# Optimization experiments

Measured on AMD Instinct MI355X. Metric: run time of the kernel, lower is better.

The kernel has to match this reference:

```python
import jax, jax.numpy as jnp
import numpy as np

B = 16384           # number of visits (segments)
EMB = 128           # embedding dim (hardcoded in module)
HID = 64            # hidden layer size
DIAG_LEN, PROC_LEN, MED_LEN = 2000, 1500, 153


def setup_inputs() -> dict:
    key = jax.random.key(0)
    ks = jax.random.split(key, 12)
    diag_codes = jax.random.randint(ks[0], (262144,), 0, DIAG_LEN)
    diag_seg = jnp.sort(jax.random.randint(ks[1], (262144,), 0, B))
    proc_codes = jax.random.randint(ks[2], (131072,), 0, PROC_LEN)
    proc_seg = jnp.sort(jax.random.randint(ks[3], (131072,), 0, B))
    med_codes = jax.random.randint(ks[4], (196608,), 0, MED_LEN)
    med_seg = jnp.sort(jax.random.randint(ks[5], (196608,), 0, B))
    diag_table = jax.random.normal(ks[6], (DIAG_LEN, EMB), dtype=jnp.float32)
    proc_table = jax.random.normal(ks[7], (PROC_LEN, EMB), dtype=jnp.float32)
    med_table = jax.random.normal(ks[8], (MED_LEN, EMB), dtype=jnp.float32)
    W1 = jax.random.normal(ks[9], (3 * EMB, HID), dtype=jnp.float32) * 0.05
    b1 = jnp.zeros((HID,), dtype=jnp.float32)
    W2 = jax.random.normal(ks[10], (HID, MED_LEN), dtype=jnp.float32) * 0.1
    b2 = jnp.zeros((MED_LEN,), dtype=jnp.float32)
    return {
        "diag_codes": diag_codes, "diag_seg": diag_seg,
        "proc_codes": proc_codes, "proc_seg": proc_seg,
        "med_codes": med_codes, "med_seg": med_seg,
        "diag_table": diag_table, "proc_table": proc_table, "med_table": med_table,
        "W1": W1, "b1": b1, "W2": W2, "b2": b2,
    }


def _embed_sum(table, codes, seg):
    # gather [N, EMB] then segment-sum to [B, EMB] (== per-visit sum of embeddings)
    return jax.ops.segment_sum(table[codes], seg, num_segments=B)


def reference(diag_codes, diag_seg, proc_codes, proc_seg, med_codes, med_seg,
              diag_table, proc_table, med_table, W1, b1, W2, b2):
    e_diag = _embed_sum(diag_table, diag_codes, diag_seg)   # [B, 128]
    e_proc = _embed_sum(proc_table, proc_codes, proc_seg)   # [B, 128]
    e_med = _embed_sum(med_table, med_codes, med_seg)       # [B, 128]
    x = jnp.concatenate([e_diag, e_proc, e_med], axis=1)    # [B, 384]
    h = jax.nn.relu(x @ W1 + b1)                            # [B, 64]
    return jax.nn.sigmoid(h @ W2 + b2)                      # [B, med_len]
```

## Files before the change

kernel.cpp:

```cpp
#include <hip/hip_runtime.h>
#include <hip/hip_bf16.h>

#define NVIS 16384
#define EMB 128
#define HID 64
#define MED 153
#define K1 384
#define VPB 16
#define NTHR 512
#define NBLK (NVIS / VPB)
#define CAPD 640
#define CAPP 384
#define CAPM 512
#define CAPT (CAPD + CAPP + CAPM)

#define W1F_OFF 0u
#define W2F_OFF 49152u
#define DIAG_OFF 69632u
#define PROC_OFF 581632u
#define MED_OFF  965632u
#define WS_NEED  1004800u

#define TQ_D 32000
#define TQ_P 24000
#define TQ_M 2448
#define TQ_ALL (TQ_D + TQ_P + TQ_M)
#define NW1F 3072
#define NW2F 1280
#define PREP_THREADS (TQ_ALL + NW1F + NW2F)
#define PREP_BLOCKS ((PREP_THREADS + 255) / 256)

typedef float f32x4 __attribute__((ext_vector_type(4)));
typedef short s16x8 __attribute__((ext_vector_type(8)));
typedef unsigned int u32;
typedef unsigned int u32x4 __attribute__((ext_vector_type(4)));

__device__ __forceinline__ unsigned short f2bf(float f) {
  union { float f; unsigned u; } v; v.f = f;
  unsigned r = v.u + 0x7FFFu + ((v.u >> 16) & 1u);
  return (unsigned short)(r >> 16);
}

__device__ __forceinline__ void acc8(u32x4 t, float& a0, float& a1, float& a2, float& a3,
                                               float& a4, float& a5, float& a6, float& a7) {
  union { unsigned u; float f; } c;
  c.u = t[0] << 16;          a0 += c.f;
  c.u = t[0] & 0xFFFF0000u;  a1 += c.f;
  c.u = t[1] << 16;          a2 += c.f;
  c.u = t[1] & 0xFFFF0000u;  a3 += c.f;
  c.u = t[2] << 16;          a4 += c.f;
  c.u = t[2] & 0xFFFF0000u;  a5 += c.f;
  c.u = t[3] << 16;          a6 += c.f;
  c.u = t[3] & 0xFFFF0000u;  a7 += c.f;
}

__device__ __forceinline__ int lb_scalar(const int* __restrict__ a, int lo, int hi, int key) {
  while (lo < hi) {
    int mid = (lo + hi) >> 1;
    if (a[mid] < key) lo = mid + 1; else hi = mid;
  }
  return lo;
}

__device__ __forceinline__ int lb_fast_scalar(const int* __restrict__ a, int n, int key) {
  long long g = ((long long)key * (long long)n) >> 14;
  int L = (int)g - 3072, R = (int)g + 3072;
  if (L < 0) L = 0;
  if (R > n) R = n;
  const bool ok = (L == 0 || a[L - 1] < key) && (R == n || a[R] >= key);
  if (!ok) { L = 0; R = n; }
  return lb_scalar(a, L, R, key);
}

__device__ __forceinline__ int lb_wave(const int* __restrict__ a, int n, int key, int lane) {
  long long g = ((long long)key * (long long)n) >> 14;
  int L = (int)g - 3072, R = (int)g + 3072;
  if (L < 0) L = 0;
  if (R > n) R = n;
  const bool ok = (L == 0 || a[L - 1] < key) && (R == n || a[R] >= key);
  if (!ok) { L = 0; R = n; }
  int lo = L - 1, hi = R;
  while (hi - lo > 1) {
    const int width = hi - lo - 1;
    const int p = lo + 1 + (int)(((long long)width * lane) >> 6);
    const bool lt = a[p] < key;
    const unsigned long long m = __ballot(lt);
    const int t = m ? (63 - __builtin_clzll(m)) : -1;
    const int nlo = (t >= 0) ? lo + 1 + (int)(((long long)width * t) >> 6) : lo;
    const int nhi = (t < 63) ? lo + 1 + (int)(((long long)width * (t + 1)) >> 6) : hi;
    lo = nlo; hi = nhi;
  }
  return hi;
}

__global__ __launch_bounds__(256, 8) void prep_kernel(
    const float* __restrict__ dT, const float* __restrict__ pT, const float* __restrict__ mT,
    const float* __restrict__ W1, const float* __restrict__ W2,
    unsigned char* __restrict__ ws)
{
  const int t = blockIdx.x * 256 + threadIdx.x;
  if (t < TQ_ALL) {
    const float* src; unsigned char* dst; int q;
    if (t < TQ_D)             { src = dT; dst = ws + DIAG_OFF; q = t; }
    else if (t < TQ_D + TQ_P) { src = pT; dst = ws + PROC_OFF; q = t - TQ_D; }
    else                      { src = mT; dst = ws + MED_OFF;  q = t - TQ_D - TQ_P; }
    const f32x4 a = *(const f32x4*)(src + (size_t)q * 8);
    const f32x4 b = *(const f32x4*)(src + (size_t)q * 8 + 4);
    u32x4 o;
    o[0] = (u32)f2bf(a[0]) | ((u32)f2bf(a[1]) << 16);
    o[1] = (u32)f2bf(a[2]) | ((u32)f2bf(a[3]) << 16);
    o[2] = (u32)f2bf(b[0]) | ((u32)f2bf(b[1]) << 16);
    o[3] = (u32)f2bf(b[2]) | ((u32)f2bf(b[3]) << 16);
    *(u32x4*)(dst + (size_t)q * 16) = o;
  } else if (t < TQ_ALL + NW1F) {
    const int idx = t - TQ_ALL;
    const int lane = idx & 63, wk = idx >> 6;
    const int kt = wk % 12, wv = wk / 12;
    const int j1 = wv * 16 + (lane & 15);
    const int kb = kt * 32 + (lane >> 4) * 8;
    unsigned short e0[8];
    #pragma unroll
    for (int e = 0; e < 8; ++e) e0[e] = f2bf(W1[(size_t)(kb + e) * HID + j1]);
    u32x4 o;
    o[0] = (u32)e0[0] | ((u32)e0[1] << 16);
    o[1] = (u32)e0[2] | ((u32)e0[3] << 16);
    o[2] = (u32)e0[4] | ((u32)e0[5] << 16);
    o[3] = (u32)e0[6] | ((u32)e0[7] << 16);
    *(u32x4*)(ws + W1F_OFF + (size_t)idx * 16) = o;
  } else if (t < TQ_ALL + NW1F + NW2F) {
    const int idx = t - TQ_ALL - NW1F;
    const int lane = idx & 63, tk = idx >> 6;
    const int kh = tk & 1, tile = tk >> 1;
    const int n = tile * 16 + (lane & 15);
    const int k0 = kh * 32 + (lane >> 4) * 8;
    unsigned short e0[8];
    #pragma unroll
    for (int e = 0; e < 8; ++e)
      e0[e] = (n < MED) ? f2bf(W2[(size_t)(k0 + e) * MED + n]) : (unsigned short)0;
    u32x4 o;
    o[0] = (u32)e0[0] | ((u32)e0[1] << 16);
    o[1] = (u32)e0[2] | ((u32)e0[3] << 16);
    o[2] = (u32)e0[4] | ((u32)e0[5] << 16);
    o[3] = (u32)e0[6] | ((u32)e0[7] << 16);
    *(u32x4*)(ws + W2F_OFF + (size_t)idx * 16) = o;
  }
}

__global__ __launch_bounds__(NTHR, 8) void fused_ehr_v5(
    const int* __restrict__ diag_codes, const int* __restrict__ diag_seg,
    const int* __restrict__ proc_codes, const int* __restrict__ proc_seg,
    const int* __restrict__ med_codes,  const int* __restrict__ med_seg,
    const float* __restrict__ b1, const float* __restrict__ b2,
    const unsigned char* __restrict__ ws,
    float* __restrict__ out, int ND, int NP, int NM)
{
  __shared__ __align__(16) unsigned short xs[VPB][K1 + 8];
  __shared__ __align__(16) unsigned short hs[VPB][HID + 8];
  __shared__ int offs[3][VPB + 1];
  __shared__ int codesL[CAPT];

  const int tid = threadIdx.x;
  const int l = tid & 63;
  const int wv = tid >> 6;
  const int b0 = blockIdx.x * VPB;

  if (wv < 6) {
    const int T = wv >> 1, w = wv & 1;
    const int* seg = (T == 0) ? diag_seg : (T == 1) ? proc_seg : med_seg;
    const int n = (T == 0) ? ND : (T == 1) ? NP : NM;
    const int r = lb_wave(seg, n, b0 + (w ? VPB : 0), l);
    if (l == 0) offs[T][w ? VPB : 0] = r;
  }
  __syncthreads();

  const int sD = offs[0][0], cntD = offs[0][VPB] - sD;
  const int sP = offs[1][0], cntP = offs[1][VPB] - sP;
  const int sM = offs[2][0], cntM = offs[2][VPB] - sM;
  const bool stD = (cntD <= CAPD), stP = (cntP <= CAPP), stM = (cntM <= CAPM);

  if (tid < 3 * (VPB - 1)) {
    const int T = tid / (VPB - 1), idx = tid - T * (VPB - 1) + 1;
    offs[T][idx] = offs[T][VPB];
  }
  if (stD) for (int i = tid; i < cntD; i += NTHR) codesL[i] = diag_codes[sD + i];
  if (stP) for (int i = tid; i < cntP; i += NTHR) codesL[CAPD + i] = proc_codes[sP + i];
  if (stM) for (int i = tid; i < cntM; i += NTHR) codesL[CAPD + CAPP + i] = med_codes[sM + i];
  __syncthreads();

#define MARK(Tidx, STAGED, CNT, SBASE, SEGG, NT)                                 \
  if (STAGED) {                                                                  \
    for (int i = tid; i < CNT; i += NTHR) {                                      \
      const int v1 = SEGG[SBASE + i];                                            \
      const int v0_ = (i == 0) ? (b0 - 1) : SEGG[SBASE + i - 1];                 \
      int klo = v0_ + 1; if (klo < b0 + 1) klo = b0 + 1;                         \
      int khi = v1;      if (khi > b0 + VPB - 1) khi = b0 + VPB - 1;             \
      for (int k = klo; k <= khi; ++k) offs[Tidx][k - b0] = SBASE + i;           \
    }                                                                            \
  } else if (tid < VPB - 1) {                                                    \
    offs[Tidx][tid + 1] = lb_fast_scalar(SEGG, NT, b0 + tid + 1);                \
  }

  MARK(0, stD, cntD, sD, diag_seg, ND)
  MARK(1, stP, cntP, sP, proc_seg, NP)
  MARK(2, stM, cntM, sM, med_seg,  NM)
#undef MARK
  __syncthreads();

  const int half = tid >> 5;
  const int ln = tid & 31;
  const int pr = ln >> 4;
  const int dd = ln & 15;
  const unsigned char* tblD = ws + DIAG_OFF;
  const unsigned char* tblP = ws + PROC_OFF;
  const unsigned char* tblM = ws + MED_OFF;

#define GATHB(T, CODES_G, TBLB, STAGED, SGLOB, LBASE)                             \
  {                                                                               \
    const int s_ = offs[T][half], e_ = offs[T][half + 1];                         \
    float a0=0.f,a1=0.f,a2=0.f,a3=0.f,a4=0.f,a5=0.f,a6=0.f,a7=0.f;                \
    int i = s_;                                                                   \
    if (STAGED) {                                                                 \
      const int lb = LBASE - SGLOB;                                               \
      for (; i + 7 < e_; i += 8) {                                                \
        const int c0 = codesL[lb + i + pr],     c1 = codesL[lb + i + 2 + pr];     \
        const int c2 = codesL[lb + i + 4 + pr], c3 = codesL[lb + i + 6 + pr];     \
        const u32x4 t0 = *(const u32x4*)(TBLB + ((size_t)c0 << 8) + (dd << 4));   \
        const u32x4 t1 = *(const u32x4*)(TBLB + ((size_t)c1 << 8) + (dd << 4));   \
        const u32x4 t2 = *(const u32x4*)(TBLB + ((size_t)c2 << 8) + (dd << 4));   \
        const u32x4 t3 = *(const u32x4*)(TBLB + ((size_t)c3 << 8) + (dd << 4));   \
        acc8(t0, a0,a1,a2,a3,a4,a5,a6,a7);                                        \
        acc8(t1, a0,a1,a2,a3,a4,a5,a6,a7);                                        \
        acc8(t2, a0,a1,a2,a3,a4,a5,a6,a7);                                        \
        acc8(t3, a0,a1,a2,a3,a4,a5,a6,a7);                                        \
      }                                                                           \
      for (; i + pr < e_; i += 2) {                                               \
        const int c = codesL[lb + i + pr];                                        \
        const u32x4 t = *(const u32x4*)(TBLB + ((size_t)c << 8) + (dd << 4));     \
        acc8(t, a0,a1,a2,a3,a4,a5,a6,a7);                                         \
      }                                                                           \
    } else {                                                                      \
      for (; i + pr < e_; i += 2) {                                               \
        const int c = CODES_G[i + pr];                                            \
        const u32x4 t = *(const u32x4*)(TBLB + ((size_t)c << 8) + (dd << 4));     \
        acc8(t, a0,a1,a2,a3,a4,a5,a6,a7);                                         \
      }                                                                           \
    }                                                                             \
    a0 += __shfl_xor(a0, 16); a1 += __shfl_xor(a1, 16);                           \
    a2 += __shfl_xor(a2, 16); a3 += __shfl_xor(a3, 16);                           \
    a4 += __shfl_xor(a4, 16); a5 += __shfl_xor(a5, 16);                           \
    a6 += __shfl_xor(a6, 16); a7 += __shfl_xor(a7, 16);                           \
    if (pr == 0) {                                                                \
      u32x4 o;                                                                    \
      o[0] = (u32)f2bf(a0) | ((u32)f2bf(a1) << 16);                               \
      o[1] = (u32)f2bf(a2) | ((u32)f2bf(a3) << 16);                               \
      o[2] = (u32)f2bf(a4) | ((u32)f2bf(a5) << 16);                               \
      o[3] = (u32)f2bf(a6) | ((u32)f2bf(a7) << 16);                               \
      *(u32x4*)&xs[half][T * EMB + dd * 8] = o;                                   \
    }                                                                             \
  }

  GATHB(0, diag_codes, tblD, stD, sD, 0)
  GATHB(1, proc_codes, tblP, stP, sP, CAPD)
  GATHB(2, med_codes,  tblM, stM, sM, CAPD + CAPP)
#undef GATHB
  __syncthreads();

  const int jloc = l & 15;
  const int kq = l >> 4;
  const s16x8* w1f = (const s16x8*)(ws + W1F_OFF);
  const s16x8* w2f = (const s16x8*)(ws + W2F_OFF);

  if (wv < 4) {
    const int j1 = wv * 16 + jloc;
    f32x4 acc = {0.f, 0.f, 0.f, 0.f};
    #pragma unroll
    for (int kt = 0; kt < 12; ++kt) {
      const s16x8 bf = w1f[(wv * 12 + kt) * 64 + l];
      const s16x8 a0 = *(const s16x8*)&xs[jloc][kt * 32 + kq * 8];
      acc = __builtin_amdgcn_mfma_f32_16x16x32_bf16(a0, bf, acc, 0, 0, 0);
    }
    const float bias1 = b1[j1];
    #pragma unroll
    for (int r = 0; r < 4; ++r)
      hs[kq * 4 + r][j1] = f2bf(fmaxf(acc[r] + bias1, 0.f));
  }
  __syncthreads();

  for (int t = wv; t < 10; t += 8) {
    const int n = t * 16 + jloc;
    const bool nok = (n < MED);
    const s16x8 bw0 = w2f[(t * 2 + 0) * 64 + l];
    const s16x8 bw1 = w2f[(t * 2 + 1) * 64 + l];
    f32x4 o0 = {0.f, 0.f, 0.f, 0.f};
    {
      const int ko = kq * 8;
      const s16x8 a00 = *(const s16x8*)&hs[jloc][ko];
      o0 = __builtin_amdgcn_mfma_f32_16x16x32_bf16(a00, bw0, o0, 0, 0, 0);
      const s16x8 a01 = *(const s16x8*)&hs[jloc][ko + 32];
      o0 = __builtin_amdgcn_mfma_f32_16x16x32_bf16(a01, bw1, o0, 0, 0, 0);
    }
    if (nok) {
      const float bias2 = b2[n];
      #pragma unroll
      for (int r = 0; r < 4; ++r) {
        const int row = kq * 4 + r;
        const float z0 = o0[r] + bias2;
        out[(size_t)(b0 + row) * MED + n] = 1.f / (1.f + __expf(-z0));
      }
    }
  }
}

__global__ __launch_bounds__(NTHR, 8) void fused_ehr_fb(
    const int* __restrict__ diag_codes, const int* __restrict__ diag_seg,
    const int* __restrict__ proc_codes, const int* __restrict__ proc_seg,
    const int* __restrict__ med_codes,  const int* __restrict__ med_seg,
    const float* __restrict__ diag_table, const float* __restrict__ proc_table,
    const float* __restrict__ med_table,
    const float* __restrict__ W1, const float* __restrict__ b1,
    const float* __restrict__ W2, const float* __restrict__ b2,
    float* __restrict__ out, int ND, int NP, int NM)
{
  __shared__ __align__(16) unsigned short xs[VPB][K1 + 8];
  __shared__ __align__(16) unsigned short hs[VPB][HID + 8];
  __shared__ int offs[3][VPB + 1];
  __shared__ int codesL[CAPT];

  const int tid = threadIdx.x;
  const int l = tid & 63;
  const int wv = tid >> 6;
  const int b0 = blockIdx.x * VPB;

  if (wv < 6) {
    const int T = wv >> 1, w = wv & 1;
    const int* seg = (T == 0) ? diag_seg : (T == 1) ? proc_seg : med_seg;
    const int n = (T == 0) ? ND : (T == 1) ? NP : NM;
    const int r = lb_wave(seg, n, b0 + (w ? VPB : 0), l);
    if (l == 0) offs[T][w ? VPB : 0] = r;
  }
  __syncthreads();

  const int sD = offs[0][0], cntD = offs[0][VPB] - sD;
  const int sP = offs[1][0], cntP = offs[1][VPB] - sP;
  const int sM = offs[2][0], cntM = offs[2][VPB] - sM;
  const bool stD = (cntD <= CAPD), stP = (cntP <= CAPP), stM = (cntM <= CAPM);

  if (tid < 3 * (VPB - 1)) {
    const int T = tid / (VPB - 1), idx = tid - T * (VPB - 1) + 1;
    offs[T][idx] = offs[T][VPB];
  }
  if (stD) for (int i = tid; i < cntD; i += NTHR) codesL[i] = diag_codes[sD + i];
  if (stP) for (int i = tid; i < cntP; i += NTHR) codesL[CAPD + i] = proc_codes[sP + i];
  if (stM) for (int i = tid; i < cntM; i += NTHR) codesL[CAPD + CAPP + i] = med_codes[sM + i];
  __syncthreads();

#define MARK(Tidx, STAGED, CNT, SBASE, SEGG, NT)                                 \
  if (STAGED) {                                                                  \
    for (int i = tid; i < CNT; i += NTHR) {                                      \
      const int v1 = SEGG[SBASE + i];                                            \
      const int v0_ = (i == 0) ? (b0 - 1) : SEGG[SBASE + i - 1];                 \
      int klo = v0_ + 1; if (klo < b0 + 1) klo = b0 + 1;                         \
      int khi = v1;      if (khi > b0 + VPB - 1) khi = b0 + VPB - 1;             \
      for (int k = klo; k <= khi; ++k) offs[Tidx][k - b0] = SBASE + i;           \
    }                                                                            \
  } else if (tid < VPB - 1) {                                                    \
    offs[Tidx][tid + 1] = lb_fast_scalar(SEGG, NT, b0 + tid + 1);                \
  }

  MARK(0, stD, cntD, sD, diag_seg, ND)
  MARK(1, stP, cntP, sP, proc_seg, NP)
  MARK(2, stM, cntM, sM, med_seg,  NM)
#undef MARK
  __syncthreads();

  const int half = tid >> 5;
  const int ln = tid & 31;

#define GATH(T, CODES_G, TBL, STAGED, SGLOB, LBASE)                               \
  {                                                                               \
    const int s_ = offs[T][half], e_ = offs[T][half + 1];                         \
    float a0 = 0.f, a1 = 0.f, a2 = 0.f, a3 = 0.f;                                 \
    int i = s_;                                                                   \
    if (STAGED) {                                                                 \
      const int lb = LBASE - SGLOB;                                               \
      for (; i + 3 < e_; i += 4) {                                                \
        const int c0 = codesL[lb + i],     c1 = codesL[lb + i + 1];               \
        const int c2 = codesL[lb + i + 2], c3 = codesL[lb + i + 3];               \
        const f32x4 t0 = *(const f32x4*)(TBL + (size_t)c0 * EMB + ln * 4);        \
        const f32x4 t1 = *(const f32x4*)(TBL + (size_t)c1 * EMB + ln * 4);        \
        const f32x4 t2 = *(const f32x4*)(TBL + (size_t)c2 * EMB + ln * 4);        \
        const f32x4 t3 = *(const f32x4*)(TBL + (size_t)c3 * EMB + ln * 4);        \
        a0 += (t0[0] + t1[0]) + (t2[0] + t3[0]);                                  \
        a1 += (t0[1] + t1[1]) + (t2[1] + t3[1]);                                  \
        a2 += (t0[2] + t1[2]) + (t2[2] + t3[2]);                                  \
        a3 += (t0[3] + t1[3]) + (t2[3] + t3[3]);                                  \
      }                                                                           \
      for (; i < e_; ++i) {                                                       \
        const int c = codesL[lb + i];                                             \
        const f32x4 t = *(const f32x4*)(TBL + (size_t)c * EMB + ln * 4);          \
        a0 += t[0]; a1 += t[1]; a2 += t[2]; a3 += t[3];                           \
      }                                                                           \
    } else {                                                                      \
      for (; i < e_; ++i) {                                                       \
        const int c = CODES_G[i];                                                 \
        const f32x4 t = *(const f32x4*)(TBL + (size_t)c * EMB + ln * 4);          \
        a0 += t[0]; a1 += t[1]; a2 += t[2]; a3 += t[3];                           \
      }                                                                           \
    }                                                                             \
    const u32 p0 = (u32)f2bf(a0) | ((u32)f2bf(a1) << 16);                         \
    const u32 p1 = (u32)f2bf(a2) | ((u32)f2bf(a3) << 16);                         \
    uint2* d_ = (uint2*)&xs[half][T * EMB + ln * 4];                              \
    *d_ = make_uint2(p0, p1);                                                     \
  }

  GATH(0, diag_codes, diag_table, stD, sD, 0)
  GATH(1, proc_codes, proc_table, stP, sP, CAPD)
  GATH(2, med_codes,  med_table,  stM, sM, CAPD + CAPP)
#undef GATH
  __syncthreads();

  const int jloc = l & 15;
  const int kq = l >> 4;

  if (wv < 4) {
    const int j1 = wv * 16 + jloc;
    f32x4 acc = {0.f, 0.f, 0.f, 0.f};
    s16x8 bf;
    #pragma unroll
    for (int e = 0; e < 8; ++e)
      bf[e] = (short)f2bf(W1[(size_t)(kq * 8 + e) * HID + j1]);
    #pragma unroll
    for (int kt = 0; kt < 12; ++kt) {
      s16x8 nxt;
      if (kt < 11) {
        const int kb = (kt + 1) * 32 + kq * 8;
        #pragma unroll
        for (int e = 0; e < 8; ++e)
          nxt[e] = (short)f2bf(W1[(size_t)(kb + e) * HID + j1]);
      }
      const s16x8 a0 = *(const s16x8*)&xs[jloc][kt * 32 + kq * 8];
      acc = __builtin_amdgcn_mfma_f32_16x16x32_bf16(a0, bf, acc, 0, 0, 0);
      if (kt < 11) bf = nxt;
    }
    const float bias1 = b1[j1];
    #pragma unroll
    for (int r = 0; r < 4; ++r)
      hs[kq * 4 + r][j1] = f2bf(fmaxf(acc[r] + bias1, 0.f));
  }
  __syncthreads();

  for (int t = wv; t < 10; t += 8) {
    const int n = t * 16 + jloc;
    const bool nok = (n < MED);
    s16x8 bw0, bw1;
    #pragma unroll
    for (int e = 0; e < 8; ++e) {
      const int k0 = kq * 8 + e;
      bw0[e] = nok ? (short)f2bf(W2[(size_t)k0 * MED + n])        : (short)0;
      bw1[e] = nok ? (short)f2bf(W2[(size_t)(k0 + 32) * MED + n]) : (short)0;
    }
    f32x4 o0 = {0.f, 0.f, 0.f, 0.f};
    {
      const int ko = kq * 8;
      const s16x8 a00 = *(const s16x8*)&hs[jloc][ko];
      o0 = __builtin_amdgcn_mfma_f32_16x16x32_bf16(a00, bw0, o0, 0, 0, 0);
      const s16x8 a01 = *(const s16x8*)&hs[jloc][ko + 32];
      o0 = __builtin_amdgcn_mfma_f32_16x16x32_bf16(a01, bw1, o0, 0, 0, 0);
    }
    if (nok) {
      const float bias2 = b2[n];
      #pragma unroll
      for (int r = 0; r < 4; ++r) {
        const int row = kq * 4 + r;
        const float z0 = o0[r] + bias2;
        out[(size_t)(b0 + row) * MED + n] = 1.f / (1.f + __expf(-z0));
      }
    }
  }
}

extern "C" void kernel_launch(void* const* d_in, const int* in_sizes, int n_in,
                              void* d_out, int out_size, void* d_ws, size_t ws_size,
                              hipStream_t stream) {
  const int* diag_codes = (const int*)d_in[0];
  const int* diag_seg   = (const int*)d_in[1];
  const int* proc_codes = (const int*)d_in[2];
  const int* proc_seg   = (const int*)d_in[3];
  const int* med_codes  = (const int*)d_in[4];
  const int* med_seg    = (const int*)d_in[5];
  const float* diag_table = (const float*)d_in[6];
  const float* proc_table = (const float*)d_in[7];
  const float* med_table  = (const float*)d_in[8];
  const float* W1 = (const float*)d_in[9];
  const float* b1 = (const float*)d_in[10];
  const float* W2 = (const float*)d_in[11];
  const float* b2 = (const float*)d_in[12];
  float* out = (float*)d_out;

  if (ws_size >= WS_NEED) {
    unsigned char* ws = (unsigned char*)d_ws;
    prep_kernel<<<dim3(PREP_BLOCKS), dim3(256), 0, stream>>>(
        diag_table, proc_table, med_table, W1, W2, ws);
    fused_ehr_v5<<<dim3(NBLK), dim3(NTHR), 0, stream>>>(
        diag_codes, diag_seg, proc_codes, proc_seg, med_codes, med_seg,
        b1, b2, ws, out, in_sizes[0], in_sizes[2], in_sizes[4]);
  } else {
    fused_ehr_fb<<<dim3(NBLK), dim3(NTHR), 0, stream>>>(
        diag_codes, diag_seg, proc_codes, proc_seg, med_codes, med_seg,
        diag_table, proc_table, med_table, W1, b1, W2, b2, out,
        in_sizes[0], in_sizes[2], in_sizes[4]);
  }
}
```

Before: 30.37 us.

## Precompute table@W1 projections so gather sums 64-wide hidden vectors directly

Uses linearity of segment sum and the first linear layer: prep kernel now multiplies each embedding table by its slice of W1 (fp32) producing 64-wide projected tables, and the main kernel gathers/sums those rows instead of 128-wide bf16 embeddings, then applies bias+ReLU directly. This removes the first MFMA GEMM, the xs staging buffer and a barrier, and halves per-code gathered columns. The cost is a heavier prep kernel (a dense 3653x128x64 matmul per call) and fp32 rows (256B per code, same bytes as before) with different rounding from the bf16 path.

```diff
diff --git a/kernel.cpp b/kernel.cpp
--- a/kernel.cpp
+++ b/kernel.cpp
@@ -14,21 +14,18 @@
 #define CAPM 512
 #define CAPT (CAPD + CAPP + CAPM)
 
-#define W1F_OFF 0u
-#define W2F_OFF 49152u
-#define DIAG_OFF 69632u
-#define PROC_OFF 581632u
-#define MED_OFF  965632u
-#define WS_NEED  1004800u
-
-#define TQ_D 32000
-#define TQ_P 24000
-#define TQ_M 2448
-#define TQ_ALL (TQ_D + TQ_P + TQ_M)
-#define NW1F 3072
+#define W2F_OFF 0u
+#define TWD_OFF 20480u
+#define TWP_OFF (20480u + 512000u)
+#define TWM_OFF (532480u + 384000u)
+#define WS_NEED (916480u + 39168u)
+
 #define NW2F 1280
-#define PREP_THREADS (TQ_ALL + NW1F + NW2F)
-#define PREP_BLOCKS ((PREP_THREADS + 255) / 256)
+#define TW_BLKS_D 500
+#define TW_BLKS_P 375
+#define TW_BLKS_M 39
+#define TW_BLKS (TW_BLKS_D + TW_BLKS_P + TW_BLKS_M)
+#define PREP_BLOCKS (TW_BLKS + 5)
 
 typedef float f32x4 __attribute__((ext_vector_type(4)));
 typedef short s16x8 __attribute__((ext_vector_type(8)));
@@ -39,19 +36,6 @@
   union { float f; unsigned u; } v; v.f = f;
   unsigned r = v.u + 0x7FFFu + ((v.u >> 16) & 1u);
   return (unsigned short)(r >> 16);
-}
-
-__device__ __forceinline__ void acc8(u32x4 t, float& a0, float& a1, float& a2, float& a3,
-                                               float& a4, float& a5, float& a6, float& a7) {
-  union { unsigned u; float f; } c;
-  c.u = t[0] << 16;          a0 += c.f;
-  c.u = t[0] & 0xFFFF0000u;  a1 += c.f;
-  c.u = t[1] << 16;          a2 += c.f;
-  c.u = t[1] & 0xFFFF0000u;  a3 += c.f;
-  c.u = t[2] << 16;          a4 += c.f;
-  c.u = t[2] & 0xFFFF0000u;  a5 += c.f;
-  c.u = t[3] << 16;          a6 += c.f;
-  c.u = t[3] & 0xFFFF0000u;  a7 += c.f;
 }
 
 __device__ __forceinline__ int lb_scalar(const int* __restrict__ a, int lo, int hi, int key) {
@@ -93,60 +77,58 @@
   return hi;
 }
 
-__global__ __launch_bounds__(256, 8) void prep_kernel(
+__global__ __launch_bounds__(256, 4) void prep_kernel(
     const float* __restrict__ dT, const float* __restrict__ pT, const float* __restrict__ mT,
     const float* __restrict__ W1, const float* __restrict__ W2,
     unsigned char* __restrict__ ws)
 {
-  const int t = blockIdx.x * 256 + threadIdx.x;
-  if (t < TQ_ALL) {
-    const float* src; unsigned char* dst; int q;
-    if (t < TQ_D)             { src = dT; dst = ws + DIAG_OFF; q = t; }
-    else if (t < TQ_D + TQ_P) { src = pT; dst = ws + PROC_OFF; q = t - TQ_D; }
-    else                      { src = mT; dst = ws + MED_OFF;  q = t - TQ_D - TQ_P; }
-    const f32x4 a = *(const f32x4*)(src + (size_t)q * 8);
-    const f32x4 b = *(const f32x4*)(src + (size_t)q * 8 + 4);
-    u32x4 o;
-    o[0] = (u32)f2bf(a[0]) | ((u32)f2bf(a[1]) << 16);
-    o[1] = (u32)f2bf(a[2]) | ((u32)f2bf(a[3]) << 16);
-    o[2] = (u32)f2bf(b[0]) | ((u32)f2bf(b[1]) << 16);
-    o[3] = (u32)f2bf(b[2]) | ((u32)f2bf(b[3]) << 16);
-    *(u32x4*)(dst + (size_t)q * 16) = o;
-  } else if (t < TQ_ALL + NW1F) {
-    const int idx = t - TQ_ALL;
-    const int lane = idx & 63, wk = idx >> 6;
-    const int kt = wk % 12, wv = wk / 12;
-    const int j1 = wv * 16 + (lane & 15);
-    const int kb = kt * 32 + (lane >> 4) * 8;
-    unsigned short e0[8];
-    #pragma unroll
-    for (int e = 0; e < 8; ++e) e0[e] = f2bf(W1[(size_t)(kb + e) * HID + j1]);
-    u32x4 o;
-    o[0] = (u32)e0[0] | ((u32)e0[1] << 16);
-    o[1] = (u32)e0[2] | ((u32)e0[3] << 16);
-    o[2] = (u32)e0[4] | ((u32)e0[5] << 16);
-    o[3] = (u32)e0[6] | ((u32)e0[7] << 16);
-    *(u32x4*)(ws + W1F_OFF + (size_t)idx * 16) = o;
-  } else if (t < TQ_ALL + NW1F + NW2F) {
-    const int idx = t - TQ_ALL - NW1F;
-    const int lane = idx & 63, tk = idx >> 6;
-    const int kh = tk & 1, tile = tk >> 1;
-    const int n = tile * 16 + (lane & 15);
-    const int k0 = kh * 32 + (lane >> 4) * 8;
-    unsigned short e0[8];
-    #pragma unroll
-    for (int e = 0; e < 8; ++e)
-      e0[e] = (n < MED) ? f2bf(W2[(size_t)(k0 + e) * MED + n]) : (unsigned short)0;
-    u32x4 o;
-    o[0] = (u32)e0[0] | ((u32)e0[1] << 16);
-    o[1] = (u32)e0[2] | ((u32)e0[3] << 16);
-    o[2] = (u32)e0[4] | ((u32)e0[5] << 16);
-    o[3] = (u32)e0[6] | ((u32)e0[7] << 16);
-    *(u32x4*)(ws + W2F_OFF + (size_t)idx * 16) = o;
-  }
-}
-
-__global__ __launch_bounds__(NTHR, 8) void fused_ehr_v5(
+  __shared__ float w1L[128 * 64];
+  const int blk = blockIdx.x;
+  const int tid = threadIdx.x;
+
+  if (blk < TW_BLKS) {
+    const float* tbl; int rows, r0, koff; unsigned char* dst;
+    if (blk < TW_BLKS_D)                 { tbl = dT; rows = 2000; r0 = blk * 4;                koff = 0;   dst = ws + TWD_OFF; }
+    else if (blk < TW_BLKS_D + TW_BLKS_P){ tbl = pT; rows = 1500; r0 = (blk - TW_BLKS_D) * 4;  koff = 128; dst = ws + TWP_OFF; }
+    else                                 { tbl = mT; rows = 153;  r0 = (blk - TW_BLKS_D - TW_BLKS_P) * 4; koff = 256; dst = ws + TWM_OFF; }
+    for (int i = tid; i < 128 * 64 / 4; i += 256)
+      *(f32x4*)&w1L[i * 4] = *(const f32x4*)&W1[(size_t)koff * HID + i * 4];
+    __syncthreads();
+
+    const int r = r0 + (tid >> 6);
+    const int j = tid & 63;
+    if (r < rows) {
+      float acc = 0.f;
+      #pragma unroll 8
+      for (int k4 = 0; k4 < 32; ++k4) {
+        const f32x4 t = *(const f32x4*)(tbl + (size_t)r * EMB + k4 * 4);
+        acc += t[0] * w1L[(k4 * 4 + 0) * 64 + j] + t[1] * w1L[(k4 * 4 + 1) * 64 + j]
+             + t[2] * w1L[(k4 * 4 + 2) * 64 + j] + t[3] * w1L[(k4 * 4 + 3) * 64 + j];
+      }
+      *(float*)(dst + ((size_t)r * HID + j) * 4) = acc;
+    }
+  } else {
+    const int t = (blk - TW_BLKS) * 256 + tid;
+    if (t < NW2F) {
+      const int lane = t & 63, tk = t >> 6;
+      const int kh = tk & 1, tile = tk >> 1;
+      const int n = tile * 16 + (lane & 15);
+      const int k0 = kh * 32 + (lane >> 4) * 8;
+      unsigned short e0[8];
+      #pragma unroll
+      for (int e = 0; e < 8; ++e)
+        e0[e] = (n < MED) ? f2bf(W2[(size_t)(k0 + e) * MED + n]) : (unsigned short)0;
+      u32x4 o;
+      o[0] = (u32)e0[0] | ((u32)e0[1] << 16);
+      o[1] = (u32)e0[2] | ((u32)e0[3] << 16);
+      o[2] = (u32)e0[4] | ((u32)e0[5] << 16);
+      o[3] = (u32)e0[6] | ((u32)e0[7] << 16);
+      *(u32x4*)(ws + W2F_OFF + (size_t)t * 16) = o;
+    }
+  }
+}
+
+__global__ __launch_bounds__(NTHR, 8) void fused_ehr_v6(
     const int* __restrict__ diag_codes, const int* __restrict__ diag_seg,
     const int* __restrict__ proc_codes, const int* __restrict__ proc_seg,
     const int* __restrict__ med_codes,  const int* __restrict__ med_seg,
@@ -154,7 +136,6 @@
     const unsigned char* __restrict__ ws,
     float* __restrict__ out, int ND, int NP, int NM)
 {
-  __shared__ __align__(16) unsigned short xs[VPB][K1 + 8];
   __shared__ __align__(16) unsigned short hs[VPB][HID + 8];
   __shared__ int offs[3][VPB + 1];
   __shared__ int codesL[CAPT];
@@ -210,81 +191,62 @@
   const int ln = tid & 31;
   const int pr = ln >> 4;
   const int dd = ln & 15;
-  const unsigned char* tblD = ws + DIAG_OFF;
-  const unsigned char* tblP = ws + PROC_OFF;
-  const unsigned char* tblM = ws + MED_OFF;
-
-#define GATHB(T, CODES_G, TBLB, STAGED, SGLOB, LBASE)                             \
+  const float* twD = (const float*)(ws + TWD_OFF);
+  const float* twP = (const float*)(ws + TWP_OFF);
+  const float* twM = (const float*)(ws + TWM_OFF);
+
+  float a0 = 0.f, a1 = 0.f, a2 = 0.f, a3 = 0.f;
+
+#define GTW(T, CODES_G, TW, STAGED, SGLOB, LBASE)                                 \
   {                                                                               \
     const int s_ = offs[T][half], e_ = offs[T][half + 1];                         \
-    float a0=0.f,a1=0.f,a2=0.f,a3=0.f,a4=0.f,a5=0.f,a6=0.f,a7=0.f;                \
     int i = s_;                                                                   \
     if (STAGED) {                                                                 \
       const int lb = LBASE - SGLOB;                                               \
       for (; i + 7 < e_; i += 8) {                                                \
         const int c0 = codesL[lb + i + pr],     c1 = codesL[lb + i + 2 + pr];     \
         const int c2 = codesL[lb + i + 4 + pr], c3 = codesL[lb + i + 6 + pr];     \
-        const u32x4 t0 = *(const u32x4*)(TBLB + ((size_t)c0 << 8) + (dd << 4));   \
-        const u32x4 t1 = *(const u32x4*)(TBLB + ((size_t)c1 << 8) + (dd << 4));   \
-        const u32x4 t2 = *(const u32x4*)(TBLB + ((size_t)c2 << 8) + (dd << 4));   \
-        const u32x4 t3 = *(const u32x4*)(TBLB + ((size_t)c3 << 8) + (dd << 4));   \
-        acc8(t0, a0,a1,a2,a3,a4,a5,a6,a7);                                        \
-        acc8(t1, a0,a1,a2,a3,a4,a5,a6,a7);                                        \
-        acc8(t2, a0,a1,a2,a3,a4,a5,a6,a7);                                        \
-        acc8(t3, a0,a1,a2,a3,a4,a5,a6,a7);                                        \
+        const f32x4 t0 = *(const f32x4*)(TW + (size_t)c0 * HID + dd * 4);         \
+        const f32x4 t1 = *(const f32x4*)(TW + (size_t)c1 * HID + dd * 4);         \
+        const f32x4 t2 = *(const f32x4*)(TW + (size_t)c2 * HID + dd * 4);         \
+        const f32x4 t3 = *(const f32x4*)(TW + (size_t)c3 * HID + dd * 4);         \
+        a0 += (t0[0] + t1[0]) + (t2[0] + t3[0]);                                  \
+        a1 += (t0[1] + t1[1]) + (t2[1] + t3[1]);                                  \
+        a2 += (t0[2] + t1[2]) + (t2[2] + t3[2]);                                  \
+        a3 += (t0[3] + t1[3]) + (t2[3] + t3[3]);                                  \
       }                                                                           \
       for (; i + pr < e_; i += 2) {                                               \
         const int c = codesL[lb + i + pr];                                        \
-        const u32x4 t = *(const u32x4*)(TBLB + ((size_t)c << 8) + (dd << 4));     \
-        acc8(t, a0,a1,a2,a3,a4,a5,a6,a7);                                         \
+        const f32x4 t = *(const f32x4*)(TW + (size_t)c * HID + dd * 4);           \
+        a0 += t[0]; a1 += t[1]; a2 += t[2]; a3 += t[3];                           \
       }                                                                           \
     } else {                                                                      \
       for (; i + pr < e_; i += 2) {                                               \
         const int c = CODES_G[i + pr];                                            \
-        const u32x4 t = *(const u32x4*)(TBLB + ((size_t)c << 8) + (dd << 4));     \
-        acc8(t, a0,a1,a2,a3,a4,a5,a6,a7);                                         \
+        const f32x4 t = *(const f32x4*)(TW + (size_t)c * HID + dd * 4);           \
+        a0 += t[0]; a1 += t[1]; a2 += t[2]; a3 += t[3];                           \
       }                                                                           \
     }                                                                             \
-    a0 += __shfl_xor(a0, 16); a1 += __shfl_xor(a1, 16);                           \
-    a2 += __shfl_xor(a2, 16); a3 += __shfl_xor(a3, 16);                           \
-    a4 += __shfl_xor(a4, 16); a5 += __shfl_xor(a5, 16);                           \
-    a6 += __shfl_xor(a6, 16); a7 += __shfl_xor(a7, 16);                           \
-    if (pr == 0) {                                                                \
-      u32x4 o;                                                                    \
-      o[0] = (u32)f2bf(a0) | ((u32)f2bf(a1) << 16);                               \
-      o[1] = (u32)f2bf(a2) | ((u32)f2bf(a3) << 16);                               \
-      o[2] = (u32)f2bf(a4) | ((u32)f2bf(a5) << 16);                               \
-      o[3] = (u32)f2bf(a6) | ((u32)f2bf(a7) << 16);                               \
-      *(u32x4*)&xs[half][T * EMB + dd * 8] = o;                                   \
-    }                                                                             \
-  }
-
-  GATHB(0, diag_codes, tblD, stD, sD, 0)
-  GATHB(1, proc_codes, tblP, stP, sP, CAPD)
-  GATHB(2, med_codes,  tblM, stM, sM, CAPD + CAPP)
-#undef GATHB
+  }
+
+  GTW(0, diag_codes, twD, stD, sD, 0)
+  GTW(1, proc_codes, twP, stP, sP, CAPD)
+  GTW(2, med_codes,  twM, stM, sM, CAPD + CAPP)
+#undef GTW
+
+  a0 += __shfl_xor(a0, 16); a1 += __shfl_xor(a1, 16);
+  a2 += __shfl_xor(a2, 16); a3 += __shfl_xor(a3, 16);
+  if (pr == 0) {
+    const f32x4 bb = *(const f32x4*)(b1 + dd * 4);
+    const u32 p0 = (u32)f2bf(fmaxf(a0 + bb[0], 0.f)) | ((u32)f2bf(fmaxf(a1 + bb[1], 0.f)) << 16);
+    const u32 p1 = (u32)f2bf(fmaxf(a2 + bb[2], 0.f)) | ((u32)f2bf(fmaxf(a3 + bb[3], 0.f)) << 16);
+    *(uint2*)&hs[half][dd * 4] = make_uint2(p0, p1);
+  }
   __syncthreads();
 
   const int jloc = l & 15;
   const int kq = l >> 4;
-  const s16x8* w1f = (const s16x8*)(ws + W1F_OFF);
   const s16x8* w2f = (const s16x8*)(ws + W2F_OFF);
-
-  if (wv < 4) {
-    const int j1 = wv * 16 + jloc;
-    f32x4 acc = {0.f, 0.f, 0.f, 0.f};
-    #pragma unroll
-    for (int kt = 0; kt < 12; ++kt) {
-      const s16x8 bf = w1f[(wv * 12 + kt) * 64 + l];
-      const s16x8 a0 = *(const s16x8*)&xs[jloc][kt * 32 + kq * 8];
-      acc = __builtin_amdgcn_mfma_f32_16x16x32_bf16(a0, bf, acc, 0, 0, 0);
-    }
-    const float bias1 = b1[j1];
-    #pragma unroll
-    for (int r = 0; r < 4; ++r)
-      hs[kq * 4 + r][j1] = f2bf(fmaxf(acc[r] + bias1, 0.f));
-  }
-  __syncthreads();
 
   for (int t = wv; t < 10; t += 8) {
     const int n = t * 16 + jloc;
@@ -501,7 +463,7 @@
     unsigned char* ws = (unsigned char*)d_ws;
     prep_kernel<<<dim3(PREP_BLOCKS), dim3(256), 0, stream>>>(
         diag_table, proc_table, med_table, W1, W2, ws);
-    fused_ehr_v5<<<dim3(NBLK), dim3(NTHR), 0, stream>>>(
+    fused_ehr_v6<<<dim3(NBLK), dim3(NTHR), 0, stream>>>(
         diag_codes, diag_seg, proc_codes, proc_seg, med_codes, med_seg,
         b1, b2, ws, out, in_sizes[0], in_sizes[2], in_sizes[4]);
   } else {
```

New measurement: 29.37 us. -3.3%, faster.
